# Optimization experiments

Measured on AMD Instinct MI355X. Metric: run time of the kernel, lower is better.

Reference implementation:

```python
import jax, jax.numpy as jnp
import numpy as np

EPS = 1e-5
NEG_SLOPE = 0.2
KMAX = 30
MS_LIST = (10, 20, 30)  # ms_list=[10,20] with kmax=30 appended, as in get_graph_feature


def _lrelu(h):
    return jnp.where(h > 0, h, NEG_SLOPE * h)


def _bn_eval(h, gamma, beta):
    # eval-mode BatchNorm2d with running_mean=0, running_var=1
    scale = gamma / jnp.sqrt(1.0 + EPS)
    return h * scale[None, :, None, None] + beta[None, :, None, None]


def setup_inputs() -> dict:
    key = jax.random.key(0)
    ks = jax.random.split(key, 5)
    B, C, N = 8, 3, 4096
    x = jax.random.normal(ks[0], (B, C, N), dtype=jnp.float32)
    w1 = jax.random.normal(ks[1], (64, 6), dtype=jnp.float32) * 0.2
    w2 = jax.random.normal(ks[2], (64, 64), dtype=jnp.float32) * 0.1
    wa = jax.random.normal(ks[3], (1, 64), dtype=jnp.float32) * 0.1
    return {
        "x": x,
        "w1": w1, "g1": jnp.ones((64,), jnp.float32), "b1": jnp.zeros((64,), jnp.float32),
        "w2": w2, "g2": jnp.ones((64,), jnp.float32), "b2": jnp.zeros((64,), jnp.float32),
        "wa": wa, "ba": jnp.zeros((1,), jnp.float32),
        "ga": jnp.ones((1,), jnp.float32), "bga": jnp.zeros((1,), jnp.float32),
    }


def _knn_idx(x, k):
    # x: [B, C, N]; pairwise_distance[b,i,j] = -||xi||^2 + 2 xi.xj - ||xj||^2
    xx = jnp.sum(x * x, axis=1, keepdims=True)            # [B, 1, N]
    inner = jnp.einsum('bcn,bcm->bnm', x, x)              # [B, N, N]
    pd = 2.0 * inner - xx - jnp.swapaxes(xx, 1, 2)        # [B, N, N]
    _, idx = jax.lax.top_k(pd, k)                         # [B, N, k], sorted nearest-first
    return idx


def reference(x, w1, g1, b1, w2, g2, b2, wa, ba, ga, bga):
    B, C, N = x.shape
    idx = _knn_idx(x, KMAX)                               # [B, N, KMAX]
    xt = jnp.transpose(x, (0, 2, 1))                      # [B, N, C]
    # one gather at kmax; per-scale feats are prefixes of the sorted neighbor list
    neigh = jax.vmap(lambda xb, ib: xb[ib])(xt, idx)      # [B, N, KMAX, C]

    acc = 0.0
    for k in MS_LIST:
        feat_k = neigh[:, :, :k, :]                       # [B, N, k, C]
        center = jnp.broadcast_to(xt[:, :, None, :], (B, N, k, C))
        f = jnp.concatenate([feat_k - center, center], axis=-1)   # [B, N, k, 2C]
        f = jnp.transpose(f, (0, 3, 1, 2))                # [B, 2C, N, k]

        h = _lrelu(_bn_eval(jnp.einsum('oi,bink->bonk', w1, f), g1, b1))
        h = _lrelu(_bn_eval(jnp.einsum('oi,bink->bonk', w2, h), g2, b2))
        a = jnp.einsum('oi,bink->bonk', wa, h) + ba[None, :, None, None]
        a = _lrelu(_bn_eval(a, ga, bga))                  # [B, 1, N, k]
        a = jax.nn.softmax(a, axis=-1)
        # attention-weighted neighbor pooling -> [B, 64, N]
        acc = acc + jnp.einsum('bnk,bcnk->bcn', a[:, 0], h)
    return acc / len(MS_LIST)
```

## Files before the change

kernel.cpp:

```cpp
#include <hip/hip_runtime.h>
#include <math.h>


#define NB 8
#define NPT 4096
#define KMAXK 30
#define ROWS (NB * NPT)
#define QW 4
#define SCAP 96

typedef __attribute__((ext_vector_type(8))) short short8v;
typedef __attribute__((ext_vector_type(4))) float float4v;
typedef __attribute__((ext_vector_type(2))) float float2v;

__device__ __forceinline__ unsigned long long shflx64(unsigned long long v, int m) {
  unsigned lo = (unsigned)__shfl_xor((int)(unsigned)(v & 0xFFFFFFFFull), m, 64);
  unsigned hi = (unsigned)__shfl_xor((int)(unsigned)(v >> 32), m, 64);
  return ((unsigned long long)hi << 32) | (unsigned long long)lo;
}

__device__ __forceinline__ short f2bf(float x) {
  unsigned u = __float_as_uint(x);
  return (short)((u + 0x7FFFu + ((u >> 16) & 1u)) >> 16);
}

__device__ __forceinline__ unsigned ordkey(float f) {
  const unsigned bits = __float_as_uint(f);
  return bits ^ ((unsigned)((int)bits >> 31) | 0x80000000u);
}

__device__ __forceinline__ float sbcast(float v) {
  return __int_as_float(__builtin_amdgcn_readfirstlane(__float_as_int(v)));
}

__global__ __launch_bounds__(256) void prep_kernel(const float* __restrict__ x,
                                                   const float* __restrict__ w2,
                                                   float4v* __restrict__ xq,
                                                   short8v* __restrict__ w2bf) {
  const int i = blockIdx.x * 256 + threadIdx.x;
  if (i < ROWS) {
    const int b = i >> 12, m = i & (NPT - 1);
    const float* xb = x + (size_t)b * 3 * NPT;
    const float y0 = xb[m], y1 = xb[NPT + m], y2 = xb[2 * NPT + m];
    const float xx = y0 * y0 + y1 * y1 + y2 * y2;
    xq[i] = (float4v){y0, y1, y2, xx};
  }
  if (blockIdx.x == ROWS / 256) {
#pragma unroll
    for (int u = 0; u < 2; ++u) {
      const int v = threadIdx.x * 2 + u;
      const int lane = v & 63, fi = v >> 6;
      const int kt = fi >> 2, nt = fi & 3;
      const int q = lane & 15, g = lane >> 4;
      const float* src = w2 + (nt * 16 + q) * 64 + kt * 32 + g * 8;
      short8v tt;
#pragma unroll
      for (int e = 0; e < 8; ++e) tt[e] = f2bf(src[e]);
      w2bf[v] = tt;
    }
  }
}

__global__ __launch_bounds__(256, 6) void knn_kernel(const float4v* __restrict__ xq,
                                                     int* __restrict__ knn) {
  __shared__ unsigned long long buf[4][QW][SCAP];
  const int wv = threadIdx.x >> 6;
  const int lane = threadIdx.x & 63;
  const int row0 = ((blockIdx.x << 2) + wv) * QW;
  const int b = row0 >> 12;
  const int n0 = row0 & (NPT - 1);
  const float4v* xqb = xq + ((size_t)b << 12);

  float qx[QW], qy[QW], qz[QW], qq[QW];
#pragma unroll
  for (int qi = 0; qi < QW; ++qi) {
    const float4v qv = xqb[n0 + qi];
    qx[qi] = sbcast(qv[0]);
    qy[qi] = sbcast(qv[1]);
    qz[qi] = sbcast(qv[2]);
    qq[qi] = sbcast(qv[3]);
  }
  float2v qxp[2], qyp[2], qzp[2], qqp[2];
#pragma unroll
  for (int p = 0; p < 2; ++p) {
    qxp[p] = (float2v){qx[2 * p], qx[2 * p + 1]};
    qyp[p] = (float2v){qy[2 * p], qy[2 * p + 1]};
    qzp[p] = (float2v){qz[2 * p], qz[2 * p + 1]};
    qqp[p] = (float2v){qq[2 * p], qq[2 * p + 1]};
  }

  float2v kmaxp[2];
  kmaxp[0] = (float2v){-3.0e38f, -3.0e38f};
  kmaxp[1] = (float2v){-3.0e38f, -3.0e38f};
  for (int j = 0; j < 64; ++j) {
    const float4v c = xqb[(j << 6) + lane];
    const float2v cx = (float2v){c[0], c[0]};
    const float2v cy = (float2v){c[1], c[1]};
    const float2v cz = (float2v){c[2], c[2]};
    const float2v cw = (float2v){c[3], c[3]};
#pragma unroll
    for (int p = 0; p < 2; ++p) {
      float2v inner = cx * qxp[p];
      inner = __builtin_elementwise_fma(cy, qyp[p], inner);
      inner = __builtin_elementwise_fma(cz, qzp[p], inner);
      const float2v pd = (inner + inner) - qqp[p] - cw;
      kmaxp[p] = __builtin_elementwise_max(kmaxp[p], pd);
    }
  }
  const float kmaxs[QW] = {kmaxp[0][0], kmaxp[0][1], kmaxp[1][0], kmaxp[1][1]};

  float thr[QW];
#pragma unroll
  for (int qi = 0; qi < QW; ++qi) {
    float v = kmaxs[qi];
#pragma unroll
    for (int kk = 2; kk <= 64; kk <<= 1) {
#pragma unroll
      for (int jj = 32; jj >= 1; jj >>= 1) {
        if (jj < kk) {
          const float o = __shfl_xor(v, jj, 64);
          const bool up = ((lane & kk) == 0);
          const bool takeMax = (((lane & jj) != 0) == up);
          v = takeMax ? fmaxf(v, o) : fminf(v, o);
        }
      }
    }
    thr[qi] = sbcast(__shfl(v, 34, 64)) - 1.0e-4f;
  }

  int cnt[QW];
#pragma unroll
  for (int qi = 0; qi < QW; ++qi) cnt[qi] = 0;
  for (int j = 0; j < 64; ++j) {
    const int m = (j << 6) + lane;
    const float4v c = xqb[m];
    const float2v cx = (float2v){c[0], c[0]};
    const float2v cy = (float2v){c[1], c[1]};
    const float2v cz = (float2v){c[2], c[2]};
    const float2v cw = (float2v){c[3], c[3]};
    float2v pdp[2];
#pragma unroll
    for (int p = 0; p < 2; ++p) {
      float2v inner = cx * qxp[p];
      inner = __builtin_elementwise_fma(cy, qyp[p], inner);
      inner = __builtin_elementwise_fma(cz, qzp[p], inner);
      pdp[p] = (inner + inner) - qqp[p] - cw;
    }
#pragma unroll
    for (int qi = 0; qi < QW; ++qi) {
      const float pd = pdp[qi >> 1][qi & 1];
      const bool pred = pd >= thr[qi];
      const unsigned long long mask = __ballot(pred);
      if (pred) {
        const int pos = cnt[qi] + (int)__popcll(mask & ((1ull << lane) - 1ull));
        if (pos < SCAP) {
          buf[wv][qi][pos] = ((unsigned long long)ordkey(pd) << 32) | (unsigned)(4095 - m);
        }
      }
      cnt[qi] += (int)__popcll(mask);
    }
  }

#pragma unroll 1
  for (int qi = 0; qi < QW; ++qi) {
    const int c = cnt[qi];
    const int outbase = (row0 + qi) * 32;
    if (c >= KMAXK && c <= 64) {
      unsigned long long val = (lane < c) ? buf[wv][qi][lane] : 0ull;
#pragma unroll
      for (int kk = 2; kk <= 64; kk <<= 1) {
#pragma unroll
        for (int jj = 32; jj >= 1; jj >>= 1) {
          if (jj < kk) {
            const unsigned long long o = shflx64(val, jj);
            const bool up = ((lane & kk) == 0);
            const bool takeMax = (((lane & jj) != 0) == up);
            const unsigned long long mx = val > o ? val : o;
            const unsigned long long mn = val > o ? o : val;
            val = takeMax ? mx : mn;
          }
        }
      }
      const int rank = 63 - lane;
      if (rank < KMAXK) {
        const int m = 4095 - (int)(val & 0xFFFFFFFFull);
        knn[outbase + rank] = m;
      }
    } else if (c > 64 && c <= SCAP) {
      for (int r = 0; r < KMAXK; ++r) {
        unsigned long long lmax = 0ull;
        int lpos = -1;
        for (int p = lane; p < c; p += 64) {
          const unsigned long long q2 = buf[wv][qi][p];
          if (q2 > lmax) { lmax = q2; lpos = p; }
        }
        unsigned long long g = lmax;
#pragma unroll
        for (int s = 32; s >= 1; s >>= 1) {
          const unsigned long long o = shflx64(g, s);
          g = o > g ? o : g;
        }
        const unsigned long long pm = __ballot(lmax == g && lpos >= 0);
        const int lowlane = (int)(__ffsll((unsigned long long)pm) - 1);
        if (lane == lowlane) buf[wv][qi][lpos] = 0ull;
        if (lane == 0) knn[outbase + r] = 4095 - (int)(g & 0xFFFFFFFFull);
      }
    } else {
      unsigned long long prev = ~0ull;
      for (int r = 0; r < KMAXK; ++r) {
        unsigned long long best = 0ull;
        for (int j = 0; j < 64; ++j) {
          const int m = (j << 6) + lane;
          const float4v cc = xqb[m];
          float inner = cc[0] * qx[qi];
          inner = fmaf(cc[1], qy[qi], inner);
          inner = fmaf(cc[2], qz[qi], inner);
          const float pd = 2.0f * inner - qq[qi] - cc[3];
          const unsigned long long key =
              ((unsigned long long)ordkey(pd) << 32) | (unsigned)(4095 - m);
          if (key < prev && key > best) best = key;
        }
#pragma unroll
        for (int s = 32; s >= 1; s >>= 1) {
          const unsigned long long o = shflx64(best, s);
          best = o > best ? o : best;
        }
        if (lane == 0) knn[outbase + r] = 4095 - (int)(best & 0xFFFFFFFFull);
        prev = best;
      }
    }
  }
}

__global__ __launch_bounds__(256) void pcc_mlp_mfma(
    const float4v* __restrict__ xq, const float* __restrict__ w1,
    const float* __restrict__ g1, const float* __restrict__ b1,
    const short8v* __restrict__ w2bf, const float* __restrict__ g2,
    const float* __restrict__ b2, const float* __restrict__ wa,
    const float* __restrict__ ba, const float* __restrict__ ga,
    const float* __restrict__ bga, const int* __restrict__ knn,
    float* __restrict__ out) {
  __shared__ float w1row[64][8];
  const int tid = threadIdx.x;
  const float invs = 1.0f / sqrtf(1.0f + 1e-5f);
  for (int idx = tid; idx < 512; idx += 256) {
    const int c = idx >> 3, s = idx & 7;
    float v;
    if (s < 6) v = w1[c * 6 + s];
    else if (s == 6) v = g1[c] * invs;
    else v = b1[c];
    w1row[c][s] = v;
  }
  __syncthreads();

  const int wv = tid >> 6, lane = tid & 63;
  const int q = lane & 15, g = lane >> 4;
  const int row = (blockIdx.x << 2) + wv;
  const int b = row >> 12, n = row & (NPT - 1);
  const float4v* xqb = xq + ((size_t)b << 12);

  short8v bf[2][4];
#pragma unroll
  for (int kt = 0; kt < 2; ++kt)
#pragma unroll
    for (int nt = 0; nt < 4; ++nt) bf[kt][nt] = w2bf[((kt << 2) + nt) * 64 + lane];

  float s2r[4], be2r[4], war[4];
#pragma unroll
  for (int nt = 0; nt < 4; ++nt) {
    s2r[nt] = g2[q + 16 * nt] * invs;
    be2r[nt] = b2[q + 16 * nt];
    war[nt] = wa[q + 16 * nt];
  }
  const float sa = ga[0] * invs, ba0 = ba[0], bga0 = bga[0];

  const float4v qv = xqb[n];
  const float xn0 = qv[0], xn1 = qv[1], xn2 = qv[2];

  const int j0 = knn[row * 32 + q];
  const float4v c0 = xqb[j0];
  float a1x = xn0, a1y = xn1, a1z = xn2;
  if (q < 14) {
    const int j1 = knn[row * 32 + 16 + q];
    const float4v c1 = xqb[j1];
    a1x = c1[0]; a1y = c1[1]; a1z = c1[2];
  }
  const float d0x = c0[0] - xn0, d0y = c0[1] - xn1, d0z = c0[2] - xn2;
  const float d1x = a1x - xn0, d1y = a1y - xn1, d1z = a1z - xn2;

  float4v dfr[2][4];
#pragma unroll
  for (int mt = 0; mt < 2; ++mt)
#pragma unroll
    for (int nt = 0; nt < 4; ++nt) dfr[mt][nt] = (float4v){0.f, 0.f, 0.f, 0.f};

#pragma unroll
  for (int kt = 0; kt < 2; ++kt) {
    short8v af0, af1;
#pragma unroll
    for (int e = 0; e < 8; ++e) {
      const int c = kt * 32 + g * 8 + e;
      const float4v wlo = *(const float4v*)&w1row[c][0];
      const float4v whi = *(const float4v*)&w1row[c][4];
      float h = wlo[0] * d0x;
      h = fmaf(wlo[1], d0y, h);
      h = fmaf(wlo[2], d0z, h);
      h = fmaf(wlo[3], xn0, h);
      h = fmaf(whi[0], xn1, h);
      h = fmaf(whi[1], xn2, h);
      h = fmaf(h, whi[2], whi[3]);
      h = fmaxf(h, 0.2f * h);
      af0[e] = f2bf(h);
      float h1v = wlo[0] * d1x;
      h1v = fmaf(wlo[1], d1y, h1v);
      h1v = fmaf(wlo[2], d1z, h1v);
      h1v = fmaf(wlo[3], xn0, h1v);
      h1v = fmaf(whi[0], xn1, h1v);
      h1v = fmaf(whi[1], xn2, h1v);
      h1v = fmaf(h1v, whi[2], whi[3]);
      h1v = fmaxf(h1v, 0.2f * h1v);
      af1[e] = f2bf(h1v);
    }
#pragma unroll
    for (int nt = 0; nt < 4; ++nt) {
      dfr[0][nt] = __builtin_amdgcn_mfma_f32_16x16x32_bf16(af0, bf[kt][nt], dfr[0][nt], 0, 0, 0);
      dfr[1][nt] = __builtin_amdgcn_mfma_f32_16x16x32_bf16(af1, bf[kt][nt], dfr[1][nt], 0, 0, 0);
    }
  }

  float part[2][4];
#pragma unroll
  for (int mt = 0; mt < 2; ++mt)
#pragma unroll
    for (int r = 0; r < 4; ++r) part[mt][r] = 0.f;
#pragma unroll
  for (int mt = 0; mt < 2; ++mt)
#pragma unroll
    for (int nt = 0; nt < 4; ++nt) {
      float4v d = dfr[mt][nt];
#pragma unroll
      for (int r = 0; r < 4; ++r) {
        float h2 = fmaf(d[r], s2r[nt], be2r[nt]);
        h2 = fmaxf(h2, 0.2f * h2);
        d[r] = h2;
        part[mt][r] = fmaf(war[nt], h2, part[mt][r]);
      }
      dfr[mt][nt] = d;
    }
#pragma unroll
  for (int mt = 0; mt < 2; ++mt)
#pragma unroll
    for (int r = 0; r < 4; ++r) {
      float p = part[mt][r];
      p += __shfl_xor(p, 1, 64);
      p += __shfl_xor(p, 2, 64);
      p += __shfl_xor(p, 4, 64);
      p += __shfl_xor(p, 8, 64);
      part[mt][r] = p;
    }

  const int mrow = g * 4;
  float sc0[4], sc1[4];
  float mloc = -3.0e38f;
#pragma unroll
  for (int r = 0; r < 4; ++r) {
    float a = fmaf(part[0][r] + ba0, sa, bga0);
    a = fmaxf(a, 0.2f * a);
    sc0[r] = a;
    mloc = fmaxf(mloc, a);
  }
#pragma unroll
  for (int r = 0; r < 4; ++r) {
    float a = fmaf(part[1][r] + ba0, sa, bga0);
    a = fmaxf(a, 0.2f * a);
    sc1[r] = a;
    if (mrow + r < 14) mloc = fmaxf(mloc, a);
  }
  mloc = fmaxf(mloc, __shfl_xor(mloc, 16, 64));
  mloc = fmaxf(mloc, __shfl_xor(mloc, 32, 64));

  float e0[4], e1[4];
  float l10 = 0.f, l20 = 0.f, l30 = 0.f;
#pragma unroll
  for (int r = 0; r < 4; ++r) {
    const float vv = expf(sc0[r] - mloc);
    e0[r] = vv;
    l30 += vv;
    l20 += vv;
    if (mrow + r < 10) l10 += vv;
  }
#pragma unroll
  for (int r = 0; r < 4; ++r) {
    const float vv = (mrow + r < 14) ? expf(sc1[r] - mloc) : 0.f;
    e1[r] = vv;
    l30 += vv;
    if (mrow + r < 4) l20 += vv;
  }
  l10 += __shfl_xor(l10, 16, 64); l10 += __shfl_xor(l10, 32, 64);
  l20 += __shfl_xor(l20, 16, 64); l20 += __shfl_xor(l20, 32, 64);
  l30 += __shfl_xor(l30, 16, 64); l30 += __shfl_xor(l30, 32, 64);
  const float i10 = 1.0f / l10, i20 = 1.0f / l20, i30 = 1.0f / l30;
  const float third = 1.0f / 3.0f;

  float wgt0[4], wgt1[4];
#pragma unroll
  for (int r = 0; r < 4; ++r) {
    wgt0[r] = e0[r] * (((mrow + r < 10) ? i10 : 0.f) + i20 + i30) * third;
    wgt1[r] = e1[r] * (((mrow + r < 4) ? i20 : 0.f) + i30) * third;
  }

  float acc[4] = {0.f, 0.f, 0.f, 0.f};
#pragma unroll
  for (int nt = 0; nt < 4; ++nt) {
#pragma unroll
    for (int r = 0; r < 4; ++r) {
      acc[nt] = fmaf(wgt0[r], dfr[0][nt][r], acc[nt]);
      acc[nt] = fmaf(wgt1[r], dfr[1][nt][r], acc[nt]);
    }
  }
#pragma unroll
  for (int nt = 0; nt < 4; ++nt) {
    acc[nt] += __shfl_xor(acc[nt], 16, 64);
    acc[nt] += __shfl_xor(acc[nt], 32, 64);
  }
  const float val = (g == 0) ? acc[0] : (g == 1) ? acc[1] : (g == 2) ? acc[2] : acc[3];
  out[(size_t)(b * 64 + q + 16 * g) * NPT + n] = val;
}

extern "C" void kernel_launch(void* const* d_in, const int* in_sizes, int n_in,
                              void* d_out, int out_size, void* d_ws, size_t ws_size,
                              hipStream_t stream) {
  const float* x = (const float*)d_in[0];
  const float* w1 = (const float*)d_in[1];
  const float* g1 = (const float*)d_in[2];
  const float* b1 = (const float*)d_in[3];
  const float* w2 = (const float*)d_in[4];
  const float* g2 = (const float*)d_in[5];
  const float* b2 = (const float*)d_in[6];
  const float* wa = (const float*)d_in[7];
  const float* ba = (const float*)d_in[8];
  const float* ga = (const float*)d_in[9];
  const float* bga = (const float*)d_in[10];
  float* out = (float*)d_out;

  float4v* xq = (float4v*)d_ws;
  int* knn = (int*)((char*)d_ws + ROWS * 16);
  short8v* w2bf = (short8v*)((char*)d_ws + ROWS * 16 + ROWS * 32 * 4);

  prep_kernel<<<dim3(ROWS / 256 + 1), dim3(256), 0, stream>>>(x, w2, xq, w2bf);
  knn_kernel<<<dim3(ROWS / (4 * QW)), dim3(256), 0, stream>>>(xq, knn);
  pcc_mlp_mfma<<<dim3(ROWS / 4), dim3(256), 0, stream>>>(
      xq, w1, g1, b1, w2bf, g2, b2, wa, ba, ga, bga, knn, out);
}
```

Baseline: 146.8 us.

## Batch knn candidate loads, fold BN1 into w1, use hardware bf16 pack

Result: faster. 135.5 us (-7.7%).

```diff
diff --git a/kernel.cpp b/kernel.cpp
--- a/kernel.cpp
+++ b/kernel.cpp
@@ -12,6 +12,7 @@
 typedef __attribute__((ext_vector_type(8))) short short8v;
 typedef __attribute__((ext_vector_type(4))) float float4v;
 typedef __attribute__((ext_vector_type(2))) float float2v;
+typedef __attribute__((ext_vector_type(4))) int int4v;
 
 __device__ __forceinline__ unsigned long long shflx64(unsigned long long v, int m) {
   unsigned lo = (unsigned)__shfl_xor((int)(unsigned)(v & 0xFFFFFFFFull), m, 64);
@@ -22,6 +23,12 @@
 __device__ __forceinline__ short f2bf(float x) {
   unsigned u = __float_as_uint(x);
   return (short)((u + 0x7FFFu + ((u >> 16) & 1u)) >> 16);
+}
+
+__device__ __forceinline__ int cvtpk(float lo, float hi) {
+  int r;
+  asm("v_cvt_pk_bf16_f32 %0, %1, %2" : "=v"(r) : "v"(lo), "v"(hi));
+  return r;
 }
 
 __device__ __forceinline__ unsigned ordkey(float f) {
@@ -70,6 +77,7 @@
   const int b = row0 >> 12;
   const int n0 = row0 & (NPT - 1);
   const float4v* xqb = xq + ((size_t)b << 12);
+  const float4v* pc = xqb + lane;
 
   float qx[QW], qy[QW], qz[QW], qq[QW];
 #pragma unroll
@@ -92,19 +100,25 @@
   float2v kmaxp[2];
   kmaxp[0] = (float2v){-3.0e38f, -3.0e38f};
   kmaxp[1] = (float2v){-3.0e38f, -3.0e38f};
-  for (int j = 0; j < 64; ++j) {
-    const float4v c = xqb[(j << 6) + lane];
-    const float2v cx = (float2v){c[0], c[0]};
-    const float2v cy = (float2v){c[1], c[1]};
-    const float2v cz = (float2v){c[2], c[2]};
-    const float2v cw = (float2v){c[3], c[3]};
-#pragma unroll
-    for (int p = 0; p < 2; ++p) {
-      float2v inner = cx * qxp[p];
-      inner = __builtin_elementwise_fma(cy, qyp[p], inner);
-      inner = __builtin_elementwise_fma(cz, qzp[p], inner);
-      const float2v pd = (inner + inner) - qqp[p] - cw;
-      kmaxp[p] = __builtin_elementwise_max(kmaxp[p], pd);
+  for (int j = 0; j < 64; j += 4) {
+    float4v cL[4];
+#pragma unroll
+    for (int u = 0; u < 4; ++u) cL[u] = pc[(size_t)(j + u) << 6];
+#pragma unroll
+    for (int u = 0; u < 4; ++u) {
+      const float4v c = cL[u];
+      const float2v cx = (float2v){c[0], c[0]};
+      const float2v cy = (float2v){c[1], c[1]};
+      const float2v cz = (float2v){c[2], c[2]};
+      const float2v cw = (float2v){c[3], c[3]};
+#pragma unroll
+      for (int p = 0; p < 2; ++p) {
+        float2v inner = cx * qxp[p];
+        inner = __builtin_elementwise_fma(cy, qyp[p], inner);
+        inner = __builtin_elementwise_fma(cz, qzp[p], inner);
+        const float2v pd = (inner + inner) - qqp[p] - cw;
+        kmaxp[p] = __builtin_elementwise_max(kmaxp[p], pd);
+      }
     }
   }
   const float kmaxs[QW] = {kmaxp[0][0], kmaxp[0][1], kmaxp[1][0], kmaxp[1][1]};
@@ -131,33 +145,42 @@
   int cnt[QW];
 #pragma unroll
   for (int qi = 0; qi < QW; ++qi) cnt[qi] = 0;
-  for (int j = 0; j < 64; ++j) {
-    const int m = (j << 6) + lane;
-    const float4v c = xqb[m];
-    const float2v cx = (float2v){c[0], c[0]};
-    const float2v cy = (float2v){c[1], c[1]};
-    const float2v cz = (float2v){c[2], c[2]};
-    const float2v cw = (float2v){c[3], c[3]};
-    float2v pdp[2];
-#pragma unroll
-    for (int p = 0; p < 2; ++p) {
-      float2v inner = cx * qxp[p];
-      inner = __builtin_elementwise_fma(cy, qyp[p], inner);
-      inner = __builtin_elementwise_fma(cz, qzp[p], inner);
-      pdp[p] = (inner + inner) - qqp[p] - cw;
-    }
-#pragma unroll
-    for (int qi = 0; qi < QW; ++qi) {
-      const float pd = pdp[qi >> 1][qi & 1];
-      const bool pred = pd >= thr[qi];
-      const unsigned long long mask = __ballot(pred);
-      if (pred) {
-        const int pos = cnt[qi] + (int)__popcll(mask & ((1ull << lane) - 1ull));
-        if (pos < SCAP) {
-          buf[wv][qi][pos] = ((unsigned long long)ordkey(pd) << 32) | (unsigned)(4095 - m);
-        }
-      }
-      cnt[qi] += (int)__popcll(mask);
+  for (int j = 0; j < 64; j += 4) {
+    float4v cL[4];
+#pragma unroll
+    for (int u = 0; u < 4; ++u) cL[u] = pc[(size_t)(j + u) << 6];
+    float2v pdp[4][2];
+#pragma unroll
+    for (int u = 0; u < 4; ++u) {
+      const float4v c = cL[u];
+      const float2v cx = (float2v){c[0], c[0]};
+      const float2v cy = (float2v){c[1], c[1]};
+      const float2v cz = (float2v){c[2], c[2]};
+      const float2v cw = (float2v){c[3], c[3]};
+#pragma unroll
+      for (int p = 0; p < 2; ++p) {
+        float2v inner = cx * qxp[p];
+        inner = __builtin_elementwise_fma(cy, qyp[p], inner);
+        inner = __builtin_elementwise_fma(cz, qzp[p], inner);
+        pdp[u][p] = (inner + inner) - qqp[p] - cw;
+      }
+    }
+#pragma unroll
+    for (int u = 0; u < 4; ++u) {
+      const int m = ((j + u) << 6) + lane;
+#pragma unroll
+      for (int qi = 0; qi < QW; ++qi) {
+        const float pd = pdp[u][qi >> 1][qi & 1];
+        const bool pred = pd >= thr[qi];
+        const unsigned long long mask = __ballot(pred);
+        if (pred) {
+          const int pos = cnt[qi] + (int)__popcll(mask & ((1ull << lane) - 1ull));
+          if (pos < SCAP) {
+            buf[wv][qi][pos] = ((unsigned long long)ordkey(pd) << 32) | (unsigned)(4095 - m);
+          }
+        }
+        cnt[qi] += (int)__popcll(mask);
+      }
     }
   }
 
@@ -240,16 +263,15 @@
     const float* __restrict__ ba, const float* __restrict__ ga,
     const float* __restrict__ bga, const int* __restrict__ knn,
     float* __restrict__ out) {
-  __shared__ float w1row[64][8];
+  __shared__ float w1s[64][8];
   const int tid = threadIdx.x;
   const float invs = 1.0f / sqrtf(1.0f + 1e-5f);
   for (int idx = tid; idx < 512; idx += 256) {
     const int c = idx >> 3, s = idx & 7;
-    float v;
-    if (s < 6) v = w1[c * 6 + s];
-    else if (s == 6) v = g1[c] * invs;
-    else v = b1[c];
-    w1row[c][s] = v;
+    float v = 0.f;
+    if (s < 6) v = w1[c * 6 + s] * (g1[c] * invs);
+    else if (s == 6) v = b1[c];
+    w1s[c][s] = v;
   }
   __syncthreads();
 
@@ -258,21 +280,6 @@
   const int row = (blockIdx.x << 2) + wv;
   const int b = row >> 12, n = row & (NPT - 1);
   const float4v* xqb = xq + ((size_t)b << 12);
-
-  short8v bf[2][4];
-#pragma unroll
-  for (int kt = 0; kt < 2; ++kt)
-#pragma unroll
-    for (int nt = 0; nt < 4; ++nt) bf[kt][nt] = w2bf[((kt << 2) + nt) * 64 + lane];
-
-  float s2r[4], be2r[4], war[4];
-#pragma unroll
-  for (int nt = 0; nt < 4; ++nt) {
-    s2r[nt] = g2[q + 16 * nt] * invs;
-    be2r[nt] = b2[q + 16 * nt];
-    war[nt] = wa[q + 16 * nt];
-  }
-  const float sa = ga[0] * invs, ba0 = ba[0], bga0 = bga[0];
 
   const float4v qv = xqb[n];
   const float xn0 = qv[0], xn1 = qv[1], xn2 = qv[2];
@@ -296,37 +303,44 @@
 
 #pragma unroll
   for (int kt = 0; kt < 2; ++kt) {
-    short8v af0, af1;
+    short8v bfk[4];
+#pragma unroll
+    for (int nt = 0; nt < 4; ++nt) bfk[nt] = w2bf[((kt << 2) + nt) * 64 + lane];
+    float h0[8], h1r[8];
 #pragma unroll
     for (int e = 0; e < 8; ++e) {
       const int c = kt * 32 + g * 8 + e;
-      const float4v wlo = *(const float4v*)&w1row[c][0];
-      const float4v whi = *(const float4v*)&w1row[c][4];
-      float h = wlo[0] * d0x;
-      h = fmaf(wlo[1], d0y, h);
-      h = fmaf(wlo[2], d0z, h);
-      h = fmaf(wlo[3], xn0, h);
-      h = fmaf(whi[0], xn1, h);
-      h = fmaf(whi[1], xn2, h);
-      h = fmaf(h, whi[2], whi[3]);
-      h = fmaxf(h, 0.2f * h);
-      af0[e] = f2bf(h);
-      float h1v = wlo[0] * d1x;
-      h1v = fmaf(wlo[1], d1y, h1v);
-      h1v = fmaf(wlo[2], d1z, h1v);
-      h1v = fmaf(wlo[3], xn0, h1v);
-      h1v = fmaf(whi[0], xn1, h1v);
-      h1v = fmaf(whi[1], xn2, h1v);
-      h1v = fmaf(h1v, whi[2], whi[3]);
-      h1v = fmaxf(h1v, 0.2f * h1v);
-      af1[e] = f2bf(h1v);
-    }
+      const float4v wlo = *(const float4v*)&w1s[c][0];
+      const float4v whi = *(const float4v*)&w1s[c][4];
+      const float hcb = fmaf(wlo[3], xn0, fmaf(whi[0], xn1, fmaf(whi[1], xn2, whi[2])));
+      float h = fmaf(wlo[0], d0x, fmaf(wlo[1], d0y, fmaf(wlo[2], d0z, hcb)));
+      h0[e] = fmaxf(h, 0.2f * h);
+      float hb = fmaf(wlo[0], d1x, fmaf(wlo[1], d1y, fmaf(wlo[2], d1z, hcb)));
+      h1r[e] = fmaxf(hb, 0.2f * hb);
+    }
+    int4v a0i, a1i;
+#pragma unroll
+    for (int e = 0; e < 4; ++e) {
+      a0i[e] = cvtpk(h0[2 * e], h0[2 * e + 1]);
+      a1i[e] = cvtpk(h1r[2 * e], h1r[2 * e + 1]);
+    }
+    const short8v af0 = __builtin_bit_cast(short8v, a0i);
+    const short8v af1 = __builtin_bit_cast(short8v, a1i);
 #pragma unroll
     for (int nt = 0; nt < 4; ++nt) {
-      dfr[0][nt] = __builtin_amdgcn_mfma_f32_16x16x32_bf16(af0, bf[kt][nt], dfr[0][nt], 0, 0, 0);
-      dfr[1][nt] = __builtin_amdgcn_mfma_f32_16x16x32_bf16(af1, bf[kt][nt], dfr[1][nt], 0, 0, 0);
-    }
-  }
+      dfr[0][nt] = __builtin_amdgcn_mfma_f32_16x16x32_bf16(af0, bfk[nt], dfr[0][nt], 0, 0, 0);
+      dfr[1][nt] = __builtin_amdgcn_mfma_f32_16x16x32_bf16(af1, bfk[nt], dfr[1][nt], 0, 0, 0);
+    }
+  }
+
+  float s2r[4], be2r[4], war[4];
+#pragma unroll
+  for (int nt = 0; nt < 4; ++nt) {
+    s2r[nt] = g2[q + 16 * nt] * invs;
+    be2r[nt] = b2[q + 16 * nt];
+    war[nt] = wa[q + 16 * nt];
+  }
+  const float sa = ga[0] * invs, ba0 = ba[0], bga0 = bga[0];
 
   float part[2][4];
 #pragma unroll
```
